# Optimization experiments

Measured on AMD Instinct MI355X. Metric: run time of the kernel, lower is better.

Reference implementation:

```python
import jax, jax.numpy as jnp
import numpy as np

N_NODES = 100000
N_EDGES = 1200000
N_GRAPHS = 2048
NUM_SHAPE, NUM_COLOR, NUM_CLASS = 8, 8, 10
MAX_POS, EMB, HID = 20, 16, 64
IN_DIM = 3 * EMB  # 48


def setup_inputs() -> dict:
    key = jax.random.key(0)
    ks = jax.random.split(key, 14)
    x = jax.random.randint(ks[0], (N_NODES, 3), 0, NUM_SHAPE)
    edge_index = jax.random.randint(ks[1], (2, N_EDGES), 0, N_NODES)
    batch = jnp.sort(jax.random.randint(ks[2], (N_NODES,), 0, N_GRAPHS))
    s = 0.1
    return {
        'x': x, 'edge_index': edge_index, 'batch': batch, 'num_graphs': N_GRAPHS,
        'shape_emb': jax.random.normal(ks[3], (NUM_SHAPE, EMB)) * s,
        'color_emb': jax.random.normal(ks[4], (NUM_COLOR, EMB)) * s,
        'pos_emb': jax.random.normal(ks[5], (MAX_POS, EMB)) * s,
        'W1_l': jax.random.normal(ks[6], (IN_DIM, HID)) * s,
        'W1_r': jax.random.normal(ks[7], (IN_DIM, HID)) * s,
        'b1': jnp.zeros((HID,)),
        'W2_l': jax.random.normal(ks[8], (HID, HID)) * s,
        'W2_r': jax.random.normal(ks[9], (HID, HID)) * s,
        'b2': jnp.zeros((HID,)),
        'Wc': jax.random.normal(ks[10], (HID, NUM_CLASS)) * s,
        'bc': jnp.zeros((NUM_CLASS,)),
    }


def _sage(h, src, dst, W_l, W_r, b, n_nodes):
    # mean-aggregate neighbor features x[src] into dst, then linear combine with root
    agg = jax.ops.segment_sum(h[src], dst, num_segments=n_nodes)
    deg = jax.ops.segment_sum(jnp.ones((src.shape[0],), h.dtype), dst, num_segments=n_nodes)
    mean = agg / jnp.maximum(deg, 1.0)[:, None]
    return mean @ W_l + h @ W_r + b


def reference(x, edge_index, batch, num_graphs, shape_emb, color_emb, pos_emb,
              W1_l, W1_r, b1, W2_l, W2_r, b2, Wc, bc):
    n_nodes = x.shape[0]
    shp = shape_emb[x[:, 0]]
    col = color_emb[x[:, 1]]
    pos = pos_emb[jnp.clip(x[:, 2], 0, MAX_POS - 1)]
    h = jnp.concatenate([shp, col, pos], axis=-1)  # [N, 48]
    src, dst = edge_index[0], edge_index[1]
    h = jax.nn.relu(_sage(h, src, dst, W1_l, W1_r, b1, n_nodes))
    h = jax.nn.relu(_sage(h, src, dst, W2_l, W2_r, b2, n_nodes))
    # global mean pool per graph
    gsum = jax.ops.segment_sum(h, batch, num_segments=num_graphs)
    gcnt = jax.ops.segment_sum(jnp.ones((n_nodes,), h.dtype), batch, num_segments=num_graphs)
    hg = gsum / jnp.maximum(gcnt, 1.0)[:, None]
    return hg @ Wc + bc
```

## Files before the change

kernel.cpp:

```cpp
#include <hip/hip_runtime.h>

#define N_NODES 100000
#define N_EDGES 1200000
#define N_GRAPHS 2048
#define CAPA 16
#define CAPB 32
#define NBUCK 500
#define DPB 200
#define BCAP 4864
#define TILE 4096

typedef unsigned int uint;
typedef unsigned short ushort;
typedef __attribute__((ext_vector_type(8))) short short8;
typedef __attribute__((ext_vector_type(4))) float f32x4;

__device__ __forceinline__ int atomAddI(int* p, int v) {
    return __hip_atomic_fetch_add(p, v, __ATOMIC_RELAXED, __HIP_MEMORY_SCOPE_AGENT);
}
__device__ __forceinline__ int clampPos(int v) { return min(max(v, 0), 19); }
__device__ __forceinline__ uint f2bf(float f) {
    uint b = __float_as_uint(f);
    return (b + 0x7fffu + ((b >> 16) & 1u)) >> 16;
}
__device__ __forceinline__ float bfLo(uint v) { return __uint_as_float(v << 16); }
__device__ __forceinline__ float bfHi(uint v) { return __uint_as_float(v & 0xffff0000u); }
__device__ __forceinline__ int bucketOf(int d) {
    return (int)(((uint)((d >> 3) * 5243)) >> 17);
}

__global__ __launch_bounds__(256) void k_init(
    const int* __restrict__ x,
    const float* __restrict__ se, const float* __restrict__ ce,
    const float* __restrict__ pe,
    const float* __restrict__ W1l, const float* __restrict__ W1r,
    const float* __restrict__ b1,
    const float* __restrict__ W2l, const float* __restrict__ W2r,
    ushort* __restrict__ WLt, ushort* __restrict__ WstkT,
    int* __restrict__ gcur, int* __restrict__ xpk) {
    int t = blockIdx.x * 256 + threadIdx.x;
    if (t < 64 * 96) {
        int col = t / 96, k = t - (t / 96) * 96;
        float v = 0.f;
        if (k < 72) {
            int bkt = (k < 36) ? k : (k - 36);
            const float* erow; int f0;
            if (bkt < 8)       { erow = se + bkt * 16;        f0 = 0;  }
            else if (bkt < 16) { erow = ce + (bkt - 8) * 16;  f0 = 16; }
            else               { erow = pe + (bkt - 16) * 16; f0 = 32; }
            const float* W = (k < 36) ? W1l : W1r;
            float a = 0.f;
            #pragma unroll
            for (int f = 0; f < 16; ++f) a = fmaf(erow[f], W[(f0 + f) * 64 + col], a);
            v = a;
        } else if (k == 72) {
            v = b1[col];
        }
        WLt[t] = (ushort)f2bf(v);
    }
    if (t < 64 * 128) {
        int col = t >> 7, k = t & 127;
        float wv = (k < 64) ? W2r[k * 64 + col] : W2l[(k - 64) * 64 + col];
        WstkT[col * 128 + k] = (ushort)f2bf(wv);
    }
    if (t < NBUCK) gcur[t] = 0;
    for (int i = t; i < N_NODES; i += 256 * 256) {
        int xs = x[i * 3 + 0], xc = x[i * 3 + 1], xp = clampPos(x[i * 3 + 2]);
        xpk[i] = xs | (xc << 8) | (xp << 16);
    }
}

__global__ __launch_bounds__(256) void k_bin(const int* __restrict__ ei,
                                             int* __restrict__ gcur,
                                             int2* __restrict__ binned) {
    __shared__ int hist[NBUCK], offs[NBUCK], runc[NBUCK], gbase[NBUCK];
    __shared__ int2 stag[TILE];
    int tid = threadIdx.x;
    int tile_base = blockIdx.x * TILE;
    int tile_n = min(TILE, N_EDGES - tile_base);
    int n4 = tile_n >> 2;
    const int4* s4p = (const int4*)(ei + tile_base);
    const int4* d4p = (const int4*)(ei + N_EDGES + tile_base);

    for (int t = tid; t < NBUCK; t += 256) hist[t] = 0;
    __syncthreads();
    for (int k = tid; k < n4; k += 256) {
        int4 d4 = d4p[k];
        #pragma unroll
        for (int i = 0; i < 4; ++i) atomicAdd(&hist[bucketOf((&d4.x)[i])], 1);
    }
    __syncthreads();
    if (tid < 64) {
        int carry = 0;
        for (int c = 0; c < 8; ++c) {
            int idx = c * 64 + tid;
            int v = (idx < NBUCK) ? hist[idx] : 0;
            int orig = v;
            #pragma unroll
            for (int o = 1; o < 64; o <<= 1) {
                int u = __shfl_up(v, o);
                if (tid >= o) v += u;
            }
            if (idx < NBUCK) offs[idx] = carry + v - orig;
            carry += __shfl(v, 63);
        }
    }
    __syncthreads();
    for (int t = tid; t < NBUCK; t += 256) runc[t] = offs[t];
    __syncthreads();
    for (int k = tid; k < n4; k += 256) {
        int4 d4 = d4p[k];
        int4 s4 = s4p[k];
        #pragma unroll
        for (int i = 0; i < 4; ++i) {
            int b = bucketOf((&d4.x)[i]);
            int pos = atomicAdd(&runc[b], 1);
            stag[pos] = make_int2((&s4.x)[i], (&d4.x)[i]);
        }
    }
    __syncthreads();
    for (int t = tid; t < NBUCK; t += 256) gbase[t] = atomAddI(&gcur[t], hist[t]);
    __syncthreads();
    for (int i = tid; i < tile_n; i += 256) {
        int2 p = stag[i];
        int b = bucketOf(p.y);
        int o = gbase[b] + (i - offs[b]);
        if (o < BCAP) binned[(size_t)b * BCAP + o] = p;
    }
}

__global__ __launch_bounds__(256) void k_place(const int2* __restrict__ binned,
                                               const int* __restrict__ gcur,
                                               int* __restrict__ cursor,
                                               int* __restrict__ slabA,
                                               int* __restrict__ slabB) {
    __shared__ int lslab[DPB][CAPA + CAPB];
    __shared__ int lcur[DPB];
    int b = blockIdx.x;
    int tid = threadIdx.x;
    if (tid < DPB) lcur[tid] = 0;
    __syncthreads();
    int n = min(gcur[b], BCAP);
    const int2* in = binned + (size_t)b * BCAP;
    for (int i = tid; i < n; i += 256) {
        int2 p = in[i];
        int local = p.y - b * DPB;
        int slot = atomicAdd(&lcur[local], 1);
        if (slot < CAPA + CAPB) lslab[local][slot] = p.x;
    }
    __syncthreads();
    for (int i = tid; i < DPB * CAPA; i += 256)
        slabA[b * DPB * CAPA + i] = lslab[i >> 4][i & 15];
    for (int i = tid; i < DPB * CAPB; i += 256)
        slabB[b * DPB * CAPB + i] = lslab[i >> 5][CAPA + (i & 31)];
    if (tid < DPB) cursor[b * DPB + tid] = lcur[tid];
}

__device__ __forceinline__ int slabAt(const int* __restrict__ slabA,
                                      const int* __restrict__ slabB,
                                      int row, int idx) {
    return (idx < CAPA) ? slabA[row * CAPA + idx] : slabB[row * CAPB + idx - CAPA];
}

__global__ __launch_bounds__(256) void k_layer1(
    const int* __restrict__ xpk, const int* __restrict__ cursor,
    const int* __restrict__ slabA, const int* __restrict__ slabB,
    const ushort* __restrict__ WLt, uint* __restrict__ AbU) {
    __shared__ int    cnt[16][104];
    __shared__ ushort scnt[16][104];
    __shared__ float  sinv[16];
    __shared__ int    sdeg[16];
    int tid = threadIdx.x;
    int row0 = blockIdx.x * 16;
    for (int i = tid; i < 16 * 104; i += 256) cnt[i / 104][i % 104] = 0;
    if (tid < 16) {
        int dg = cursor[row0 + tid];
        sdeg[tid] = min(dg, CAPA + CAPB);
        sinv[tid] = 1.0f / fmaxf((float)dg, 1.0f);
    }
    __syncthreads();
    for (int i = tid; i < 16 * 48; i += 256) {
        int r = i / 48, idx = i - r * 48;
        if (idx < sdeg[r]) {
            int p = xpk[slabAt(slabA, slabB, row0 + r, idx)];
            atomicAdd(&cnt[r][p & 0xff], 1);
            atomicAdd(&cnt[r][8 + ((p >> 8) & 0xff)], 1);
            atomicAdd(&cnt[r][16 + (p >> 16)], 1);
        }
    }
    if (tid < 16) {
        int p0 = xpk[row0 + tid];
        cnt[tid][36 + (p0 & 0xff)] = 1;
        cnt[tid][44 + ((p0 >> 8) & 0xff)] = 1;
        cnt[tid][52 + (p0 >> 16)] = 1;
        cnt[tid][72] = 1;
    }
    __syncthreads();
    for (int i = tid; i < 16 * 96; i += 256) {
        int r = i / 96, k = i - r * 96;
        float v = (float)cnt[r][k];
        if (k < 36) v *= sinv[r];
        scnt[r][k] = (ushort)f2bf(v);
    }
    __syncthreads();
    int w = tid >> 6, lane = tid & 63;
    int lo16 = lane & 15, hi4 = lane >> 4;
    f32x4 acc = {0.f, 0.f, 0.f, 0.f};
    #pragma unroll
    for (int ks = 0; ks < 3; ++ks) {
        short8 a8 = *(const short8*)(&scnt[lo16][ks * 32 + hi4 * 8]);
        short8 b8 = *(const short8*)(WLt + (w * 16 + lo16) * 96 + ks * 32 + hi4 * 8);
        acc = __builtin_amdgcn_mfma_f32_16x16x32_bf16(a8, b8, acc, 0, 0, 0);
    }
    #pragma unroll
    for (int r = 0; r < 4; ++r) {
        uint rb = f2bf(fmaxf(acc[r], 0.0f));
        uint nxt = __shfl_down(rb, 1);
        if ((lo16 & 1) == 0) {
            int node = row0 + hi4 * 4 + r;
            AbU[(size_t)node * 64 + ((w * 16 + lo16) >> 1)] = rb | (nxt << 16);
        }
    }
}

__global__ __launch_bounds__(256) void k_g2(
    const uint* __restrict__ AbU, const int* __restrict__ cursor,
    const int* __restrict__ slabA, const int* __restrict__ slabB,
    const ushort* __restrict__ WstkT, const float* __restrict__ b2,
    uint* __restrict__ h2b) {
    __shared__ uint Ab[64][68];
    int tid = threadIdx.x;
    int row0 = blockIdx.x * 64;
    for (int i = tid; i < 64 * 32; i += 256) {
        int r = i >> 5, c = i & 31;
        int gr = min(row0 + r, N_NODES - 1);
        Ab[r][c] = AbU[(size_t)gr * 64 + c];
    }
    int w = tid >> 6, lane = tid & 63;
    int half = lane >> 5, l = lane & 31;
    for (int pr = 0; pr < 8; ++pr) {
        int lr = w * 16 + pr * 2 + half;
        int row = row0 + lr;
        int deg = 0, m = 0;
        if (row < N_NODES) { deg = cursor[row]; m = min(deg, CAPA + CAPB); }
        int nb0 = (l < m)      ? slabAt(slabA, slabB, row, l)      : 0;
        int nb1 = (l + 32 < m) ? slabB[row * CAPB + l + 32 - CAPA] : 0;
        float ax = 0.f, ay = 0.f;
        int d = 0;
        for (; d + 2 <= m; d += 2) {
            int s0 = __shfl((d < 32) ? nb0 : nb1, (half << 5) | (d & 31));
            int s1 = __shfl((d + 1 < 32) ? nb0 : nb1, (half << 5) | ((d + 1) & 31));
            uint v0 = AbU[(size_t)s0 * 64 + l];
            uint v1 = AbU[(size_t)s1 * 64 + l];
            ax += bfLo(v0) + bfLo(v1);
            ay += bfHi(v0) + bfHi(v1);
        }
        if (d < m) {
            int s = __shfl((d < 32) ? nb0 : nb1, (half << 5) | (d & 31));
            uint v = AbU[(size_t)s * 64 + l];
            ax += bfLo(v);
            ay += bfHi(v);
        }
        float inv = 1.0f / fmaxf((float)deg, 1.0f);
        Ab[lr][32 + l] = f2bf(ax * inv) | (f2bf(ay * inv) << 16);
    }
    int lo16 = lane & 15, hi4 = lane >> 4;
    short8 bfr[4][4];
    #pragma unroll
    for (int nb = 0; nb < 4; ++nb) {
        #pragma unroll
        for (int kb = 0; kb < 4; ++kb)
            bfr[nb][kb] = *(const short8*)(WstkT + (nb * 16 + lo16) * 128 + kb * 32 + hi4 * 8);
    }
    float bb[4];
    #pragma unroll
    for (int nb = 0; nb < 4; ++nb) bb[nb] = b2[nb * 16 + lo16];
    __syncthreads();
    short8 a8[4];
    #pragma unroll
    for (int kb = 0; kb < 4; ++kb)
        a8[kb] = *(const short8*)(&Ab[w * 16 + lo16][kb * 16 + hi4 * 4]);
    f32x4 acc[4] = {{0,0,0,0},{0,0,0,0},{0,0,0,0},{0,0,0,0}};
    #pragma unroll
    for (int kb = 0; kb < 4; ++kb) {
        #pragma unroll
        for (int nb = 0; nb < 4; ++nb)
            acc[nb] = __builtin_amdgcn_mfma_f32_16x16x32_bf16(a8[kb], bfr[nb][kb], acc[nb], 0, 0, 0);
    }
    #pragma unroll
    for (int nb = 0; nb < 4; ++nb) {
        #pragma unroll
        for (int r = 0; r < 4; ++r) {
            uint rb = f2bf(fmaxf(acc[nb][r] + bb[nb], 0.0f));
            uint nxt = __shfl_down(rb, 1);
            if ((lo16 & 1) == 0) {
                int orow = row0 + w * 16 + hi4 * 4 + r;
                if (orow < N_NODES)
                    h2b[(size_t)orow * 32 + ((nb * 16 + lo16) >> 1)] = rb | (nxt << 16);
            }
        }
    }
}

__device__ __forceinline__ int lowerBound(const int* __restrict__ b, int n, int v) {
    int lo = 0, hi = n;
    while (lo < hi) { int mid = (lo + hi) >> 1; if (b[mid] < v) lo = mid + 1; else hi = mid; }
    return lo;
}

__global__ __launch_bounds__(256) void k_pool_final(
    const uint* __restrict__ h2b, const int* __restrict__ batch,
    const float* __restrict__ Wc, const float* __restrict__ bc,
    float* __restrict__ out) {
    int g = blockIdx.x * 8 + (threadIdx.x >> 5);
    if (g >= N_GRAPHS) return;
    int l = threadIdx.x & 31;
    int lo = lowerBound(batch, N_NODES, g);
    int hi = lowerBound(batch, N_NODES, g + 1);
    float ax0 = 0.f, ay0 = 0.f, ax1 = 0.f, ay1 = 0.f;
    int n = lo;
    for (; n + 2 <= hi; n += 2) {
        uint v0 = h2b[(size_t)n * 32 + l];
        uint v1 = h2b[(size_t)(n + 1) * 32 + l];
        ax0 += bfLo(v0); ay0 += bfHi(v0);
        ax1 += bfLo(v1); ay1 += bfHi(v1);
    }
    if (n < hi) {
        uint v = h2b[(size_t)n * 32 + l];
        ax0 += bfLo(v); ay0 += bfHi(v);
    }
    float inv = 1.0f / fmaxf((float)(hi - lo), 1.0f);
    float mx = (ax0 + ax1) * inv, my = (ay0 + ay1) * inv;
    #pragma unroll
    for (int c = 0; c < 10; ++c) {
        float p = fmaf(mx, Wc[(2 * l) * 10 + c], my * Wc[(2 * l + 1) * 10 + c]);
        #pragma unroll
        for (int off = 16; off >= 1; off >>= 1) p += __shfl_xor(p, off);
        if (l == 0) out[g * 10 + c] = p + bc[c];
    }
}

extern "C" void kernel_launch(void* const* d_in, const int* in_sizes, int n_in,
                              void* d_out, int out_size, void* d_ws, size_t ws_size,
                              hipStream_t stream) {
    const int* x     = (const int*)d_in[0];
    const int* ei    = (const int*)d_in[1];
    const int* batch = (const int*)d_in[2];
    const float* se  = (const float*)d_in[4];
    const float* ce  = (const float*)d_in[5];
    const float* pe  = (const float*)d_in[6];
    const float* W1l = (const float*)d_in[7];
    const float* W1r = (const float*)d_in[8];
    const float* b1  = (const float*)d_in[9];
    const float* W2l = (const float*)d_in[10];
    const float* W2r = (const float*)d_in[11];
    const float* b2  = (const float*)d_in[12];
    const float* Wc  = (const float*)d_in[13];
    const float* bc  = (const float*)d_in[14];

    float* ws    = (float*)d_ws;
    uint*  AbU   = (uint*)ws;
    uint*  h2b   = (uint*)(ws + 6400000);
    int2*  binned= (int2*)ws;
    int*   slabA = (int*)(ws + 12800000);
    int*   slabB = (int*)(ws + 14400000);
    int*   cursor= (int*)(ws + 17600000);
    int*   xpk   = (int*)(ws + 17700000);
    ushort* WstkT= (ushort*)(ws + 17806000);
    ushort* WLt  = (ushort*)(ws + 17810100);
    int*   gcur  = (int*)(ws + 17814000);

    k_init<<<256, 256, 0, stream>>>(x, se, ce, pe, W1l, W1r, b1, W2l, W2r,
                                    WLt, WstkT, gcur, xpk);
    k_bin<<<(N_EDGES + TILE - 1) / TILE, 256, 0, stream>>>(ei, gcur, binned);
    k_place<<<NBUCK, 256, 0, stream>>>(binned, gcur, cursor, slabA, slabB);
    k_layer1<<<N_NODES / 16, 256, 0, stream>>>(xpk, cursor, slabA, slabB, WLt, AbU);
    k_g2<<<(N_NODES + 63) / 64, 256, 0, stream>>>(AbU, cursor, slabA, slabB,
                                                  WstkT, b2, h2b);
    k_pool_final<<<N_GRAPHS / 8, 256, 0, stream>>>(h2b, batch, Wc, bc, (float*)d_out);
}
```

Baseline: 154.8 us.

## Split layer-2 gather and GEMM into separate kernels

The fused layer-2 kernel, which gathered neighbour means into shared memory and then ran MFMA, is split in two. A gather kernel gives each half-wavefront one node and writes the bf16 mean into the upper half of each AbU row. A separate GEMM kernel then reads whole rows straight from global memory, with no LDS staging or block barrier. This aims to let the latency-bound gather run at full occupancy without the shared-memory and barrier limits. The cost is an extra launch and a global-memory round trip for the mean features.

```diff
diff --git a/kernel.cpp b/kernel.cpp
--- a/kernel.cpp
+++ b/kernel.cpp
@@ -223,47 +223,43 @@
     }
 }
 
-__global__ __launch_bounds__(256) void k_g2(
-    const uint* __restrict__ AbU, const int* __restrict__ cursor,
-    const int* __restrict__ slabA, const int* __restrict__ slabB,
-    const ushort* __restrict__ WstkT, const float* __restrict__ b2,
-    uint* __restrict__ h2b) {
-    __shared__ uint Ab[64][68];
-    int tid = threadIdx.x;
-    int row0 = blockIdx.x * 64;
-    for (int i = tid; i < 64 * 32; i += 256) {
-        int r = i >> 5, c = i & 31;
-        int gr = min(row0 + r, N_NODES - 1);
-        Ab[r][c] = AbU[(size_t)gr * 64 + c];
-    }
-    int w = tid >> 6, lane = tid & 63;
+__global__ __launch_bounds__(256) void k_gather(
+    uint* __restrict__ AbU, const int* __restrict__ cursor,
+    const int* __restrict__ slabA, const int* __restrict__ slabB) {
+    int gid = blockIdx.x * 256 + threadIdx.x;
+    int wid = gid >> 6;
+    int lane = threadIdx.x & 63;
     int half = lane >> 5, l = lane & 31;
-    for (int pr = 0; pr < 8; ++pr) {
-        int lr = w * 16 + pr * 2 + half;
-        int row = row0 + lr;
-        int deg = 0, m = 0;
-        if (row < N_NODES) { deg = cursor[row]; m = min(deg, CAPA + CAPB); }
-        int nb0 = (l < m)      ? slabAt(slabA, slabB, row, l)      : 0;
-        int nb1 = (l + 32 < m) ? slabB[row * CAPB + l + 32 - CAPA] : 0;
-        float ax = 0.f, ay = 0.f;
-        int d = 0;
-        for (; d + 2 <= m; d += 2) {
-            int s0 = __shfl((d < 32) ? nb0 : nb1, (half << 5) | (d & 31));
-            int s1 = __shfl((d + 1 < 32) ? nb0 : nb1, (half << 5) | ((d + 1) & 31));
-            uint v0 = AbU[(size_t)s0 * 64 + l];
-            uint v1 = AbU[(size_t)s1 * 64 + l];
-            ax += bfLo(v0) + bfLo(v1);
-            ay += bfHi(v0) + bfHi(v1);
-        }
-        if (d < m) {
-            int s = __shfl((d < 32) ? nb0 : nb1, (half << 5) | (d & 31));
-            uint v = AbU[(size_t)s * 64 + l];
-            ax += bfLo(v);
-            ay += bfHi(v);
-        }
-        float inv = 1.0f / fmaxf((float)deg, 1.0f);
-        Ab[lr][32 + l] = f2bf(ax * inv) | (f2bf(ay * inv) << 16);
-    }
+    int row = wid * 2 + half;
+    if (row >= N_NODES) return;
+    int deg = cursor[row];
+    int m = min(deg, CAPA + CAPB);
+    int nb0 = (l < m)      ? slabAt(slabA, slabB, row, l)      : 0;
+    int nb1 = (l + 32 < m) ? slabB[row * CAPB + l + 32 - CAPA] : 0;
+    float ax = 0.f, ay = 0.f;
+    int d = 0;
+    for (; d + 2 <= m; d += 2) {
+        int s0 = __shfl((d < 32) ? nb0 : nb1, (half << 5) | (d & 31));
+        int s1 = __shfl((d + 1 < 32) ? nb0 : nb1, (half << 5) | ((d + 1) & 31));
+        uint v0 = AbU[(size_t)s0 * 64 + l];
+        uint v1 = AbU[(size_t)s1 * 64 + l];
+        ax += bfLo(v0) + bfLo(v1);
+        ay += bfHi(v0) + bfHi(v1);
+    }
+    if (d < m) {
+        int s = __shfl((d < 32) ? nb0 : nb1, (half << 5) | (d & 31));
+        uint v = AbU[(size_t)s * 64 + l];
+        ax += bfLo(v);
+        ay += bfHi(v);
+    }
+    float inv = 1.0f / fmaxf((float)deg, 1.0f);
+    AbU[(size_t)row * 64 + 32 + l] = f2bf(ax * inv) | (f2bf(ay * inv) << 16);
+}
+
+__global__ __launch_bounds__(256) void k_gemm(
+    const uint* __restrict__ AbU, const ushort* __restrict__ WstkT,
+    const float* __restrict__ b2, uint* __restrict__ h2b) {
+    int w = threadIdx.x >> 6, lane = threadIdx.x & 63;
     int lo16 = lane & 15, hi4 = lane >> 4;
     short8 bfr[4][4];
     #pragma unroll
@@ -275,11 +271,14 @@
     float bb[4];
     #pragma unroll
     for (int nb = 0; nb < 4; ++nb) bb[nb] = b2[nb * 16 + lo16];
-    __syncthreads();
+
+    int row0 = blockIdx.x * 64 + w * 16;
+    int arow = min(row0 + lo16, N_NODES - 1);
+    const short8* Arow = (const short8*)(AbU + (size_t)arow * 64);
     short8 a8[4];
     #pragma unroll
-    for (int kb = 0; kb < 4; ++kb)
-        a8[kb] = *(const short8*)(&Ab[w * 16 + lo16][kb * 16 + hi4 * 4]);
+    for (int kb = 0; kb < 4; ++kb) a8[kb] = Arow[kb * 4 + hi4];
+
     f32x4 acc[4] = {{0,0,0,0},{0,0,0,0},{0,0,0,0},{0,0,0,0}};
     #pragma unroll
     for (int kb = 0; kb < 4; ++kb) {
@@ -294,7 +293,7 @@
             uint rb = f2bf(fmaxf(acc[nb][r] + bb[nb], 0.0f));
             uint nxt = __shfl_down(rb, 1);
             if ((lo16 & 1) == 0) {
-                int orow = row0 + w * 16 + hi4 * 4 + r;
+                int orow = row0 + hi4 * 4 + r;
                 if (orow < N_NODES)
                     h2b[(size_t)orow * 32 + ((nb * 16 + lo16) >> 1)] = rb | (nxt << 16);
             }
@@ -375,7 +374,7 @@
     k_bin<<<(N_EDGES + TILE - 1) / TILE, 256, 0, stream>>>(ei, gcur, binned);
     k_place<<<NBUCK, 256, 0, stream>>>(binned, gcur, cursor, slabA, slabB);
     k_layer1<<<N_NODES / 16, 256, 0, stream>>>(xpk, cursor, slabA, slabB, WLt, AbU);
-    k_g2<<<(N_NODES + 63) / 64, 256, 0, stream>>>(AbU, cursor, slabA, slabB,
-                                                  WstkT, b2, h2b);
+    k_gather<<<12500, 256, 0, stream>>>(AbU, cursor, slabA, slabB);
+    k_gemm<<<(N_NODES + 63) / 64, 256, 0, stream>>>(AbU, WstkT, b2, h2b);
     k_pool_final<<<N_GRAPHS / 8, 256, 0, stream>>>(h2b, batch, Wc, bc, (float*)d_out);
 }
```

New measurement: 131.3 us. 1.18x faster.
